# Performance work log

Hardware: AMD Instinct MI355X
Metric: run time of the kernel (lower is better)

Reference implementation:

```python
import jax, jax.numpy as jnp
import numpy as np

KH, KW = 3, 3
KN = KH * KW  # kernel_n = 9


def _grid_offset(H, W):
    # Faithful to TF build(): stack(meshgrid(ij)).reshape(-1, 2) -- note this
    # interleaves i- and j- grids in an unusual layout; we replicate it exactly.
    init = jnp.stack(jnp.meshgrid(jnp.arange(KH), jnp.arange(KW), indexing='ij'))
    init = init.reshape(-1, 2).astype(jnp.float32)  # (KN, 2)
    ph, pw = (KH - 1) // 2, (KW - 1) // 2
    g = jnp.stack(
        jnp.meshgrid(jnp.arange(-ph, H - ph), jnp.arange(-pw, W - pw), indexing='ij'),
        axis=-1,
    ).astype(jnp.float32)  # (H, W, 2)
    return g[:, :, None, :] + init[None, None]  # (H, W, KN, 2)


def _bilinear_sample(x, coords):
    # x: (B, H, W, C); coords: (B, H, W, KN, 2) with (row, col) float coords.
    B = x.shape[0]
    y, xc = coords[..., 0], coords[..., 1]
    y0 = jnp.floor(y).astype(jnp.int32)
    y1 = jnp.ceil(y).astype(jnp.int32)   # ceil (not floor+1), faithful to TF code
    x0 = jnp.floor(xc).astype(jnp.int32)
    x1 = jnp.ceil(xc).astype(jnp.int32)
    bidx = jnp.arange(B)[:, None, None, None]

    def g(yy, xx):
        return x[bidx, yy, xx]  # (B, H, W, KN, C)

    v_lt = g(y0, x0)
    v_rb = g(y1, x1)
    v_lb = g(y0, x1)  # (lt_row, rb_col) per TF coords_lb
    v_rt = g(y1, x0)  # (rb_row, lt_col) per TF coords_rt
    fy = (y - y0.astype(y.dtype))[..., None]
    fx = (xc - x0.astype(xc.dtype))[..., None]
    v_t = v_lt + (v_rt - v_lt) * fy
    v_b = v_lb + (v_rb - v_lb) * fy
    return v_t + (v_b - v_t) * fx  # (B, H, W, KN, C)


def setup_inputs() -> dict:
    key = jax.random.key(0)
    k1, k2, k3 = jax.random.split(key, 3)
    B, H, W, C, F = 8, 64, 64, 128, 128
    x = jax.random.normal(k1, (B, H, W, C), dtype=jnp.float32)
    offset = jax.random.normal(k2, (B, H, W, 2 * KN), dtype=jnp.float32)
    Wk = jax.random.truncated_normal(k3, -2.0, 2.0, (KN, C, F), dtype=jnp.float32) * 0.02
    b = jnp.zeros((F,), dtype=jnp.float32)
    return {"x": x, "offset": offset, "W": Wk, "b": b}


def reference(x, offset, W, b):
    B, H, Wd, C = x.shape
    coords = _grid_offset(H, Wd)[None] + offset.reshape(B, H, Wd, KN, 2)
    coords = jnp.stack(
        [
            jnp.clip(coords[..., 0], 0.0, float(H - 1)),
            jnp.clip(coords[..., 1], 0.0, float(Wd - 1)),
        ],
        axis=-1,
    )
    deform = _bilinear_sample(x, coords)  # (B, H, W, KN, C)
    # conv3d with (1,1,KN,C,F) filter, VALID == contraction over (KN, C)
    out = jnp.einsum('bhwnc,ncf->bhwf', deform, W) + b
    return out
```

## Files before the change

### kernel.cpp

```cpp
#include <hip/hip_runtime.h>
#include <stdint.h>

#define KN 9
#define HH 64
#define WW 64
#define CC 128
#define FF 128
#define TM 64
#define NT 512
#define LDK 136

typedef __bf16 bf16x8 __attribute__((ext_vector_type(8)));
typedef float f32x4 __attribute__((ext_vector_type(4)));
typedef unsigned short us8 __attribute__((ext_vector_type(8)));
typedef unsigned short us4 __attribute__((ext_vector_type(4)));

__constant__ float c_init_i[KN] = {0.f,0.f,1.f,2.f,2.f,1.f,0.f,2.f,1.f};
__constant__ float c_init_j[KN] = {0.f,1.f,1.f,2.f,0.f,2.f,1.f,0.f,2.f};

static __device__ inline unsigned short f2bf(float f) {
    union { float f; unsigned u; } v; v.f = f;
    unsigned r = v.u + 0x7fffu + ((v.u >> 16) & 1u);
    return (unsigned short)(r >> 16);
}

__global__ void wt_kernel(const float* __restrict__ Wk, unsigned short* __restrict__ Wt) {
    __shared__ unsigned short t[32][33];
    const int tid = threadIdx.x;
    const int n  = blockIdx.x >> 4;
    const int tf = blockIdx.x & 3;
    const int tc = (blockIdx.x >> 2) & 3;
    const int g  = tid >> 5;
    const int l  = tid & 31;
#pragma unroll
    for (int r = 0; r < 4; ++r) {
        int cl = g * 4 + r;
        t[cl][l] = f2bf(Wk[(n << 14) + ((tc * 32 + cl) << 7) + (tf * 32 + l)]);
    }
    __syncthreads();
#pragma unroll
    for (int r = 0; r < 4; ++r) {
        int fl = g * 4 + r;
        Wt[(n << 14) + (tc << 12) + ((tf * 32 + fl) << 5) + l] = t[l][fl];
    }
}

#define ISSUE(n_, p_, S) do {                                          \
    int4 cb_ = *(const int4*)&cB[p_][n_][0];                           \
    lt##S = *(const float4*)(bbase + cb_.x + icg);                     \
    rt##S = *(const float4*)(bbase + cb_.y + icg);                     \
    lb##S = *(const float4*)(bbase + cb_.z + icg);                     \
    rb##S = *(const float4*)(bbase + cb_.w + icg);                     \
    __builtin_amdgcn_sched_barrier(0);                                 \
  } while (0)

#define CONSUME(n_, p_, S) do {                                        \
    float fy_ = cF[p_][n_][0], fx_ = cF[p_][n_][1];                    \
    us4 pk_;                                                           \
    _Pragma("unroll")                                                  \
    for (int j = 0; j < 4; ++j) {                                      \
      float v0_ = lt##S[j], v1_ = rt##S[j], v2_ = lb##S[j], v3_ = rb##S[j]; \
      float vt_ = v0_ + (v1_ - v0_) * fy_;                             \
      float vb_ = v2_ + (v3_ - v2_) * fy_;                             \
      float r_  = vt_ + (vb_ - vt_) * fx_;                             \
      pk_[j] = __builtin_bit_cast(unsigned short, (__bf16)r_);         \
    }                                                                  \
    *(us4*)&As[d][p_][icg] = pk_;                                      \
  } while (0)

#define MSTEP(ks_, B0, B1) do {                                        \
    bf16x8 a0_ = __builtin_bit_cast(bf16x8, *(const us8*)(&As[d][mtile + col][(ks_) * 32 + quad * 8]));      \
    bf16x8 a1_ = __builtin_bit_cast(bf16x8, *(const us8*)(&As[d][mtile + 16 + col][(ks_) * 32 + quad * 8])); \
    acc00 = __builtin_amdgcn_mfma_f32_16x16x32_bf16(a0_, __builtin_bit_cast(bf16x8, B0), acc00, 0, 0, 0);    \
    acc01 = __builtin_amdgcn_mfma_f32_16x16x32_bf16(a0_, __builtin_bit_cast(bf16x8, B1), acc01, 0, 0, 0);    \
    acc10 = __builtin_amdgcn_mfma_f32_16x16x32_bf16(a1_, __builtin_bit_cast(bf16x8, B0), acc10, 0, 0, 0);    \
    acc11 = __builtin_amdgcn_mfma_f32_16x16x32_bf16(a1_, __builtin_bit_cast(bf16x8, B1), acc11, 0, 0, 0);    \
  } while (0)

__launch_bounds__(NT, 4)
__global__ void deform_kernel(const float* __restrict__ xin,
                              const float* __restrict__ off,
                              const unsigned short* __restrict__ Wt,
                              const float* __restrict__ bias,
                              float* __restrict__ out) {
    __shared__ unsigned short As[2][TM][LDK];
    __shared__ int   cB[TM][KN][4];
    __shared__ float cF[TM][KN][2];

    const int tid = threadIdx.x;
    const int bb   = blockIdx.x & 7;
    const int hh   = blockIdx.x >> 3;
    const int pix0 = (bb << 12) + (hh << 6);

    for (int t = tid; t < TM * KN; t += NT) {
        int p = t & (TM - 1);
        int n = t >> 6;
        float2 o = *(const float2*)(off + (size_t)(pix0 + p) * (2 * KN) + 2 * n);
        float y = (float)(hh - 1) + c_init_i[n] + o.x;
        float x = (float)(p - 1) + c_init_j[n] + o.y;
        y = fminf(fmaxf(y, 0.f), 63.f);
        x = fminf(fmaxf(x, 0.f), 63.f);
        float y0f = floorf(y), x0f = floorf(x);
        int y0 = (int)y0f, x0 = (int)x0f;
        int y1 = (int)ceilf(y), x1 = (int)ceilf(x);
        cB[p][n][0] = ((y0 << 6) + x0) << 7;
        cB[p][n][1] = ((y1 << 6) + x0) << 7;
        cB[p][n][2] = ((y0 << 6) + x1) << 7;
        cB[p][n][3] = ((y1 << 6) + x1) << 7;
        cF[p][n][0] = y - y0f;
        cF[p][n][1] = x - x0f;
    }

    const int wave = tid >> 6;
    const int lane = tid & 63;
    const int quad = lane >> 4;
    const int col  = lane & 15;
    const int mtile = (wave & 1) * 32;
    const int ntile = (wave >> 1) * 32;

    f32x4 acc00 = {0.f,0.f,0.f,0.f}, acc01 = {0.f,0.f,0.f,0.f};
    f32x4 acc10 = {0.f,0.f,0.f,0.f}, acc11 = {0.f,0.f,0.f,0.f};

    const float* bbase = xin + ((size_t)bb << 19);
    const unsigned short* wb0 = Wt + ((ntile + col) << 5) + (quad << 3);

    const int ip  = tid >> 5;
    const int icg = (tid & 31) * 4;

    float4 ltA, rtA, lbA, rbA;
    float4 ltB, rtB, lbB, rbB;
    us8 bfr0, bfr1, bfr2, bfr3, bfr4, bfr5, bfr6, bfr7;

    __syncthreads();

    int d = 0;
    ISSUE(0, ip, A);

    for (int n = 0; n < KN; ++n, d ^= 1) {
        const unsigned short* wn = wb0 + (n << 14);
        bfr0 = *(const us8*)(wn);
        bfr1 = *(const us8*)(wn + 512);
        bfr2 = *(const us8*)(wn + 4096);
        bfr3 = *(const us8*)(wn + 4096 + 512);
        bfr4 = *(const us8*)(wn + 8192);
        bfr5 = *(const us8*)(wn + 8192 + 512);
        bfr6 = *(const us8*)(wn + 12288);
        bfr7 = *(const us8*)(wn + 12288 + 512);
        __builtin_amdgcn_sched_barrier(0);

        ISSUE(n, ip + 16, B);
        CONSUME(n, ip, A);
        ISSUE(n, ip + 32, A);
        CONSUME(n, ip + 16, B);
        ISSUE(n, ip + 48, B);
        CONSUME(n, ip + 32, A);
        CONSUME(n, ip + 48, B);

        asm volatile("s_waitcnt lgkmcnt(0)" ::: "memory");
        __builtin_amdgcn_s_barrier();

        if (n + 1 < KN) ISSUE(n + 1, ip, A);

        MSTEP(0, bfr0, bfr1);
        MSTEP(1, bfr2, bfr3);
        MSTEP(2, bfr4, bfr5);
        MSTEP(3, bfr6, bfr7);
    }

#pragma unroll
    for (int b = 0; b < 2; ++b) {
        int f = ntile + b * 16 + col;
        float bv = bias[f];
        const f32x4 ac0 = b ? acc01 : acc00;
        const f32x4 ac1 = b ? acc11 : acc10;
#pragma unroll
        for (int r = 0; r < 4; ++r) {
            int pr0 = pix0 + mtile + quad * 4 + r;
            out[(size_t)pr0 * FF + f] = ac0[r] + bv;
            int pr1 = pr0 + 16;
            out[(size_t)pr1 * FF + f] = ac1[r] + bv;
        }
    }
}

extern "C" void kernel_launch(void* const* d_in, const int* in_sizes, int n_in,
                              void* d_out, int out_size, void* d_ws, size_t ws_size,
                              hipStream_t stream) {
    const float* x    = (const float*)d_in[0];
    const float* off  = (const float*)d_in[1];
    const float* Wk   = (const float*)d_in[2];
    const float* bias = (const float*)d_in[3];
    float* out = (float*)d_out;
    unsigned short* Wt = (unsigned short*)d_ws;

    wt_kernel<<<KN * 16, 256, 0, stream>>>(Wk, Wt);
    deform_kernel<<<(8 * HH * WW) / TM, NT, 0, stream>>>(x, off, Wt, bias, out);
}
```

Baseline: 112.3 us.

## Pre-convert input to bf16 and stage weights into LDS via async loads

Adds a pre-pass that converts x to bf16 in workspace, so each bilinear corner gather moves half the bytes and each thread handles eight channels. Weights are pre-swizzled into an MFMA-friendly layout and copied directly into LDS with global_load_lds each tap, replacing per-wave register loads. Corner offsets are packed as two ints, and the A tile is single-buffered with an extra barrier. The cost is an extra kernel launch plus a full read and write of x, more LDS use that may lower occupancy, and x is now rounded to bf16 before interpolation, which lowers precision.

```diff
diff --git a/kernel.cpp b/kernel.cpp
--- a/kernel.cpp
+++ b/kernel.cpp
@@ -13,15 +13,28 @@
 typedef __bf16 bf16x8 __attribute__((ext_vector_type(8)));
 typedef float f32x4 __attribute__((ext_vector_type(4)));
 typedef unsigned short us8 __attribute__((ext_vector_type(8)));
-typedef unsigned short us4 __attribute__((ext_vector_type(4)));
 
 __constant__ float c_init_i[KN] = {0.f,0.f,1.f,2.f,2.f,1.f,0.f,2.f,1.f};
 __constant__ float c_init_j[KN] = {0.f,1.f,1.f,2.f,0.f,2.f,1.f,0.f,2.f};
 
-static __device__ inline unsigned short f2bf(float f) {
-    union { float f; unsigned u; } v; v.f = f;
-    unsigned r = v.u + 0x7fffu + ((v.u >> 16) & 1u);
-    return (unsigned short)(r >> 16);
+static __device__ inline float bf2f(unsigned short u) {
+    union { unsigned u; float f; } v; v.u = ((unsigned)u) << 16; return v.f;
+}
+
+__global__ void xb_kernel(const float* __restrict__ x, unsigned short* __restrict__ xb) {
+    int i = (blockIdx.x * 256 + threadIdx.x) * 8;
+    float4 a = *(const float4*)(x + i);
+    float4 b = *(const float4*)(x + i + 4);
+    us8 o;
+    o[0] = __builtin_bit_cast(unsigned short, (__bf16)a.x);
+    o[1] = __builtin_bit_cast(unsigned short, (__bf16)a.y);
+    o[2] = __builtin_bit_cast(unsigned short, (__bf16)a.z);
+    o[3] = __builtin_bit_cast(unsigned short, (__bf16)a.w);
+    o[4] = __builtin_bit_cast(unsigned short, (__bf16)b.x);
+    o[5] = __builtin_bit_cast(unsigned short, (__bf16)b.y);
+    o[6] = __builtin_bit_cast(unsigned short, (__bf16)b.z);
+    o[7] = __builtin_bit_cast(unsigned short, (__bf16)b.w);
+    *(us8*)(xb + i) = o;
 }
 
 __global__ void wt_kernel(const float* __restrict__ Wk, unsigned short* __restrict__ Wt) {
@@ -35,56 +48,82 @@
 #pragma unroll
     for (int r = 0; r < 4; ++r) {
         int cl = g * 4 + r;
-        t[cl][l] = f2bf(Wk[(n << 14) + ((tc * 32 + cl) << 7) + (tf * 32 + l)]);
+        t[cl][l] = __builtin_bit_cast(unsigned short,
+                    (__bf16)Wk[(n << 14) + ((tc * 32 + cl) << 7) + (tf * 32 + l)]);
     }
     __syncthreads();
 #pragma unroll
     for (int r = 0; r < 4; ++r) {
-        int fl = g * 4 + r;
-        Wt[(n << 14) + (tc << 12) + ((tf * 32 + fl) << 5) + l] = t[l][fl];
-    }
-}
-
-#define ISSUE(n_, p_, S) do {                                          \
-    int4 cb_ = *(const int4*)&cB[p_][n_][0];                           \
-    lt##S = *(const float4*)(bbase + cb_.x + icg);                     \
-    rt##S = *(const float4*)(bbase + cb_.y + icg);                     \
-    lb##S = *(const float4*)(bbase + cb_.z + icg);                     \
-    rb##S = *(const float4*)(bbase + cb_.w + icg);                     \
+        int o   = r * 256 + tid;
+        int b   = o >> 9;
+        int q   = (o >> 7) & 3;
+        int col = (o >> 3) & 15;
+        int e   = o & 7;
+        Wt[(((n * 4 + tc) * 4 + tf) << 10) + o] = t[q * 8 + e][b * 16 + col];
+    }
+}
+
+#define ISSUE(n_, s_, S) do {                                          \
+    int p_ = (s_) >> 4; int ch_ = ((s_) & 15) * 8;                     \
+    int lt_o = cB[p_][n_][0], rb_o = cB[p_][n_][1];                    \
+    int rt_o = (rb_o & 0x7E000) | (lt_o & 0x1F80);                     \
+    int lb_o = (lt_o & 0x7E000) | (rb_o & 0x1F80);                     \
+    lt##S = *(const us8*)(bb16 + lt_o + ch_);                          \
+    rt##S = *(const us8*)(bb16 + rt_o + ch_);                          \
+    lb##S = *(const us8*)(bb16 + lb_o + ch_);                          \
+    rb##S = *(const us8*)(bb16 + rb_o + ch_);                          \
     __builtin_amdgcn_sched_barrier(0);                                 \
   } while (0)
 
-#define CONSUME(n_, p_, S) do {                                        \
+#define CONSUME(n_, s_, S) do {                                        \
+    int p_ = (s_) >> 4; int ch_ = ((s_) & 15) * 8;                     \
     float fy_ = cF[p_][n_][0], fx_ = cF[p_][n_][1];                    \
-    us4 pk_;                                                           \
+    us8 pk_;                                                           \
     _Pragma("unroll")                                                  \
-    for (int j = 0; j < 4; ++j) {                                      \
-      float v0_ = lt##S[j], v1_ = rt##S[j], v2_ = lb##S[j], v3_ = rb##S[j]; \
+    for (int j = 0; j < 8; ++j) {                                      \
+      float v0_ = bf2f(lt##S[j]), v1_ = bf2f(rt##S[j]);                \
+      float v2_ = bf2f(lb##S[j]), v3_ = bf2f(rb##S[j]);                \
       float vt_ = v0_ + (v1_ - v0_) * fy_;                             \
       float vb_ = v2_ + (v3_ - v2_) * fy_;                             \
       float r_  = vt_ + (vb_ - vt_) * fx_;                             \
       pk_[j] = __builtin_bit_cast(unsigned short, (__bf16)r_);         \
     }                                                                  \
-    *(us4*)&As[d][p_][icg] = pk_;                                      \
-  } while (0)
-
-#define MSTEP(ks_, B0, B1) do {                                        \
-    bf16x8 a0_ = __builtin_bit_cast(bf16x8, *(const us8*)(&As[d][mtile + col][(ks_) * 32 + quad * 8]));      \
-    bf16x8 a1_ = __builtin_bit_cast(bf16x8, *(const us8*)(&As[d][mtile + 16 + col][(ks_) * 32 + quad * 8])); \
-    acc00 = __builtin_amdgcn_mfma_f32_16x16x32_bf16(a0_, __builtin_bit_cast(bf16x8, B0), acc00, 0, 0, 0);    \
-    acc01 = __builtin_amdgcn_mfma_f32_16x16x32_bf16(a0_, __builtin_bit_cast(bf16x8, B1), acc01, 0, 0, 0);    \
-    acc10 = __builtin_amdgcn_mfma_f32_16x16x32_bf16(a1_, __builtin_bit_cast(bf16x8, B0), acc10, 0, 0, 0);    \
-    acc11 = __builtin_amdgcn_mfma_f32_16x16x32_bf16(a1_, __builtin_bit_cast(bf16x8, B1), acc11, 0, 0, 0);    \
+    *(us8*)&As[p_][ch_] = pk_;                                         \
+  } while (0)
+
+#define MSTEP(ks_) do {                                                \
+    bf16x8 a0_ = __builtin_bit_cast(bf16x8, *(const us8*)(&As[mtile + col][(ks_) * 32 + quad * 8]));      \
+    bf16x8 a1_ = __builtin_bit_cast(bf16x8, *(const us8*)(&As[mtile + 16 + col][(ks_) * 32 + quad * 8])); \
+    bf16x8 b0_ = __builtin_bit_cast(bf16x8, *(const us8*)(&Bt[(((ks_) * 4 + gi) * 2 + 0) * 512 + lane * 8])); \
+    bf16x8 b1_ = __builtin_bit_cast(bf16x8, *(const us8*)(&Bt[(((ks_) * 4 + gi) * 2 + 1) * 512 + lane * 8])); \
+    acc00 = __builtin_amdgcn_mfma_f32_16x16x32_bf16(a0_, b0_, acc00, 0, 0, 0);    \
+    acc01 = __builtin_amdgcn_mfma_f32_16x16x32_bf16(a0_, b1_, acc01, 0, 0, 0);    \
+    acc10 = __builtin_amdgcn_mfma_f32_16x16x32_bf16(a1_, b0_, acc10, 0, 0, 0);    \
+    acc11 = __builtin_amdgcn_mfma_f32_16x16x32_bf16(a1_, b1_, acc11, 0, 0, 0);    \
+  } while (0)
+
+typedef __attribute__((address_space(3))) unsigned int lds_u32;
+typedef __attribute__((address_space(1))) const unsigned int glb_u32;
+#define STAGE_BT(n_) do {                                              \
+    const unsigned int* src_ = (const unsigned int*)(Wt + ((size_t)(n_) << 14)); \
+    _Pragma("unroll")                                                  \
+    for (int r_ = 0; r_ < 4; ++r_) {                                   \
+      __builtin_amdgcn_global_load_lds(                                \
+          (glb_u32*)(src_ + (r_ << 11) + (wave << 8) + (lane << 2)),   \
+          (lds_u32*)((unsigned int*)Bt + (r_ << 11) + (wave << 8)),    \
+          16, 0, 0);                                                   \
+    }                                                                  \
   } while (0)
 
 __launch_bounds__(NT, 4)
-__global__ void deform_kernel(const float* __restrict__ xin,
+__global__ void deform_kernel(const unsigned short* __restrict__ xb,
                               const float* __restrict__ off,
                               const unsigned short* __restrict__ Wt,
                               const float* __restrict__ bias,
                               float* __restrict__ out) {
-    __shared__ unsigned short As[2][TM][LDK];
-    __shared__ int   cB[TM][KN][4];
+    __shared__ unsigned short As[TM][LDK];
+    __shared__ unsigned short Bt[16384];
+    __shared__ int   cB[TM][KN][2];
     __shared__ float cF[TM][KN][2];
 
     const int tid = threadIdx.x;
@@ -103,10 +142,8 @@
         float y0f = floorf(y), x0f = floorf(x);
         int y0 = (int)y0f, x0 = (int)x0f;
         int y1 = (int)ceilf(y), x1 = (int)ceilf(x);
-        cB[p][n][0] = ((y0 << 6) + x0) << 7;
-        cB[p][n][1] = ((y1 << 6) + x0) << 7;
-        cB[p][n][2] = ((y0 << 6) + x1) << 7;
-        cB[p][n][3] = ((y1 << 6) + x1) << 7;
+        cB[p][n][0] = (y0 << 13) | (x0 << 7);
+        cB[p][n][1] = (y1 << 13) | (x1 << 7);
         cF[p][n][0] = y - y0f;
         cF[p][n][1] = x - x0f;
     }
@@ -117,54 +154,36 @@
     const int col  = lane & 15;
     const int mtile = (wave & 1) * 32;
     const int ntile = (wave >> 1) * 32;
+    const int gi    = wave >> 1;
 
     f32x4 acc00 = {0.f,0.f,0.f,0.f}, acc01 = {0.f,0.f,0.f,0.f};
     f32x4 acc10 = {0.f,0.f,0.f,0.f}, acc11 = {0.f,0.f,0.f,0.f};
 
-    const float* bbase = xin + ((size_t)bb << 19);
-    const unsigned short* wb0 = Wt + ((ntile + col) << 5) + (quad << 3);
-
-    const int ip  = tid >> 5;
-    const int icg = (tid & 31) * 4;
-
-    float4 ltA, rtA, lbA, rbA;
-    float4 ltB, rtB, lbB, rbB;
-    us8 bfr0, bfr1, bfr2, bfr3, bfr4, bfr5, bfr6, bfr7;
+    const unsigned short* bb16 = xb + ((size_t)bb << 19);
+
+    us8 ltA, rtA, lbA, rbA;
+    us8 ltB, rtB, lbB, rbB;
 
     __syncthreads();
 
-    int d = 0;
-    ISSUE(0, ip, A);
-
-    for (int n = 0; n < KN; ++n, d ^= 1) {
-        const unsigned short* wn = wb0 + (n << 14);
-        bfr0 = *(const us8*)(wn);
-        bfr1 = *(const us8*)(wn + 512);
-        bfr2 = *(const us8*)(wn + 4096);
-        bfr3 = *(const us8*)(wn + 4096 + 512);
-        bfr4 = *(const us8*)(wn + 8192);
-        bfr5 = *(const us8*)(wn + 8192 + 512);
-        bfr6 = *(const us8*)(wn + 12288);
-        bfr7 = *(const us8*)(wn + 12288 + 512);
-        __builtin_amdgcn_sched_barrier(0);
-
-        ISSUE(n, ip + 16, B);
-        CONSUME(n, ip, A);
-        ISSUE(n, ip + 32, A);
-        CONSUME(n, ip + 16, B);
-        ISSUE(n, ip + 48, B);
-        CONSUME(n, ip + 32, A);
-        CONSUME(n, ip + 48, B);
-
-        asm volatile("s_waitcnt lgkmcnt(0)" ::: "memory");
+    STAGE_BT(0);
+    ISSUE(0, tid, A);
+
+    for (int n = 0; n < KN; ++n) {
+        ISSUE(n, tid + NT, B);
+        CONSUME(n, tid, A);
+        CONSUME(n, tid + NT, B);
+        __syncthreads();
+
+        if (n + 1 < KN) ISSUE(n + 1, tid, A);
+
+        MSTEP(0);
+        MSTEP(1);
+        MSTEP(2);
+        MSTEP(3);
+
         __builtin_amdgcn_s_barrier();
-
-        if (n + 1 < KN) ISSUE(n + 1, ip, A);
-
-        MSTEP(0, bfr0, bfr1);
-        MSTEP(1, bfr2, bfr3);
-        MSTEP(2, bfr4, bfr5);
-        MSTEP(3, bfr6, bfr7);
+        if (n + 1 < KN) STAGE_BT(n + 1);
     }
 
 #pragma unroll
@@ -192,7 +211,9 @@
     const float* bias = (const float*)d_in[3];
     float* out = (float*)d_out;
     unsigned short* Wt = (unsigned short*)d_ws;
-
+    unsigned short* xb = (unsigned short*)d_ws + 147456;
+
+    xb_kernel<<<2048, 256, 0, stream>>>(x, xb);
     wt_kernel<<<KN * 16, 256, 0, stream>>>(Wk, Wt);
-    deform_kernel<<<(8 * HH * WW) / TM, NT, 0, stream>>>(x, off, Wt, bias, out);
-}
+    deform_kernel<<<(8 * HH * WW) / TM, NT, 0, stream>>>(xb, off, Wt, bias, out);
+}
```

Result: faster. 101.1 us (-10.0%).
